# Kernel tuning notes

Measured on AMD Instinct MI355X. Metric: run time of the kernel, lower is better.

## Reference

```python
import jax, jax.numpy as jnp
import numpy as np


def _gcn_conv(x, src, dst, W, b, n_nodes):
    # PyG GCNConv: add self-loops, symmetric deg^{-1/2} normalization, then linear.
    xw = x @ W  # [N, H]
    # degree including self-loop (count of incoming edges at dst + 1)
    deg = jnp.zeros((n_nodes,), dtype=xw.dtype).at[dst].add(1.0) + 1.0
    dinv = jax.lax.rsqrt(deg)  # deg >= 1 always
    coef = (dinv[src] * dinv[dst])[:, None]  # [E, 1]
    out = jnp.zeros_like(xw).at[dst].add(xw[src] * coef)
    # self-loop edge i->i has norm dinv[i]^2
    out = out + xw * (dinv * dinv)[:, None]
    return out + b


def setup_inputs() -> dict:
    key = jax.random.key(0)
    ks = jax.random.split(key, 6)
    N, E, F, H, G = 200000, 600000, 128, 128, 64
    x = jax.random.normal(ks[0], (N, F), dtype=jnp.float32)
    edge_index = jax.random.randint(ks[1], (2, E), 0, N, dtype=jnp.int64)
    batch = jnp.sort(jax.random.randint(ks[2], (N,), 0, G, dtype=jnp.int64))
    W1 = jax.random.normal(ks[3], (F, H), dtype=jnp.float32) * (1.0 / np.sqrt(F))
    b1 = jnp.zeros((H,), dtype=jnp.float32)
    W2 = jax.random.normal(ks[4], (H, H), dtype=jnp.float32) * (1.0 / np.sqrt(H))
    b2 = jnp.zeros((H,), dtype=jnp.float32)
    return {"x": x, "edge_index": edge_index, "batch": batch, "num_graphs": G,
            "W1": W1, "b1": b1, "W2": W2, "b2": b2}


def reference(x, edge_index, batch, num_graphs, W1, b1, W2, b2):
    n_nodes = x.shape[0]
    # feature standardization (torch .std is unbiased, ddof=1)
    x = (x - x.mean(axis=0, keepdims=True)) / x.std(axis=0, keepdims=True, ddof=1)
    src, dst = edge_index[0], edge_index[1]
    h = jax.nn.relu(_gcn_conv(x, src, dst, W1, b1, n_nodes))
    # dropout p=0 -> identity
    h = jax.nn.relu(_gcn_conv(h, src, dst, W2, b2, n_nodes))
    # global_add_pool over batch ids
    return jax.ops.segment_sum(h, batch, num_segments=num_graphs)
```

## Files before the change

kernel.cpp:

```cpp
#include <hip/hip_runtime.h>

#define FDIM 128

typedef __attribute__((ext_vector_type(8))) short short8;
typedef __attribute__((ext_vector_type(4))) float f32x4;

__device__ inline unsigned short f2bf(float f) {
    unsigned int u = __float_as_uint(f);
    unsigned int r = u + 0x7FFFu + ((u >> 16) & 1u);
    return (unsigned short)(r >> 16);
}
__device__ inline float bf2f(unsigned short b) {
    return __uint_as_float((unsigned int)b << 16);
}
__device__ inline void bf8_fma(short8 v, float c, float* acc) {
#pragma unroll
    for (int k = 0; k < 8; ++k)
        acc[k] = fmaf(bf2f(((const unsigned short*)&v)[k]), c, acc[k]);
}

__global__ __launch_bounds__(256) void col_stats_kernel(const float* __restrict__ x, int N,
                                                        float* __restrict__ partials) {
    const int c4 = threadIdx.x & 31;
    const int rg = threadIdx.x >> 5;
    float4 s = make_float4(0.f, 0.f, 0.f, 0.f);
    float4 q = make_float4(0.f, 0.f, 0.f, 0.f);
    for (long r = (long)blockIdx.x * 8 + rg; r < N; r += (long)gridDim.x * 8) {
        float4 v = ((const float4*)x)[r * 32 + c4];
        s.x += v.x; s.y += v.y; s.z += v.z; s.w += v.w;
        q.x += v.x * v.x; q.y += v.y * v.y; q.z += v.z * v.z; q.w += v.w * v.w;
    }
    __shared__ float red[8][32][8];
    float* p = red[rg][c4];
    p[0] = s.x; p[1] = s.y; p[2] = s.z; p[3] = s.w;
    p[4] = q.x; p[5] = q.y; p[6] = q.z; p[7] = q.w;
    __syncthreads();
    if (rg == 0) {
#pragma unroll
        for (int g = 1; g < 8; ++g) {
            const float* o = red[g][c4];
#pragma unroll
            for (int j = 0; j < 8; ++j) red[0][c4][j] += o[j];
        }
        const float* r0 = red[0][c4];
        float* out = &partials[(size_t)blockIdx.x * 256];
        ((float4*)out)[c4] = make_float4(r0[0], r0[1], r0[2], r0[3]);
        ((float4*)(out + 128))[c4] = make_float4(r0[4], r0[5], r0[6], r0[7]);
    }
}

__global__ __launch_bounds__(1024) void finalize_stats(const float* __restrict__ partials,
                                                       int nblk, int N,
                                                       float* __restrict__ mean,
                                                       float* __restrict__ rstd) {
    __shared__ float sh[8][2][FDIM];
    int g = threadIdx.x >> 7;
    int j = threadIdx.x & 127;
    float s = 0.f, q = 0.f;
    for (int b = g; b < nblk; b += 8) {
        s += partials[(size_t)b * 256 + j];
        q += partials[(size_t)b * 256 + 128 + j];
    }
    sh[g][0][j] = s;
    sh[g][1][j] = q;
    __syncthreads();
    if (g == 0) {
#pragma unroll
        for (int k = 1; k < 8; ++k) { s += sh[k][0][j]; q += sh[k][1][j]; }
        float m = s / (float)N;
        float var = (q - (float)N * m * m) / (float)(N - 1);
        mean[j] = m;
        rstd[j] = rsqrtf(var);
    }
}

__global__ void prep_wt(const float* __restrict__ W1, const float* __restrict__ W2,
                        const float* __restrict__ mean, const float* __restrict__ rstd,
                        unsigned short* __restrict__ WT1, unsigned short* __restrict__ WT2,
                        float* __restrict__ bias0) {
    int h = threadIdx.x;
    int b = blockIdx.x;
    if (b < 8) {
        float acc = 0.f;
#pragma unroll
        for (int jj = 0; jj < 16; ++jj) {
            int j = b * 16 + jj;
            float w = W1[j * FDIM + h] * rstd[j];
            WT1[h * FDIM + j] = f2bf(w);
            acc += mean[j] * w;
        }
        unsafeAtomicAdd(&bias0[h], -acc);
    } else {
#pragma unroll
        for (int jj = 0; jj < 16; ++jj) {
            int j = (b - 8) * 16 + jj;
            WT2[h * FDIM + j] = f2bf(W2[j * FDIM + h]);
        }
    }
}

__global__ void deg_count(const int* __restrict__ dst, int E, int* __restrict__ cnt) {
    int e = blockIdx.x * blockDim.x + threadIdx.x;
    if (e < E) atomicAdd(&cnt[dst[e]], 1);
}

__global__ __launch_bounds__(256) void alloc_offsets(const int* __restrict__ cnt, int N,
                                                     int* __restrict__ start,
                                                     int* __restrict__ wcur,
                                                     int* __restrict__ counter,
                                                     float* __restrict__ dinv) {
    __shared__ int sh[256];
    __shared__ int base;
    int i = blockIdx.x * 256 + threadIdx.x;
    int v = (i < N) ? cnt[i] : 0;
    sh[threadIdx.x] = v;
    __syncthreads();
    for (int off = 1; off < 256; off <<= 1) {
        int t = (threadIdx.x >= off) ? sh[threadIdx.x - off] : 0;
        __syncthreads();
        sh[threadIdx.x] += t;
        __syncthreads();
    }
    if (threadIdx.x == 255) base = atomicAdd(counter, sh[255]);
    __syncthreads();
    int excl = base + sh[threadIdx.x] - v;
    if (i < N) {
        start[i] = excl;
        wcur[i] = excl;
        dinv[i] = rsqrtf((float)v + 1.0f);
    }
}

__global__ void fill_edges(const int* __restrict__ src, const int* __restrict__ dst,
                           const float* __restrict__ dinv, int E,
                           int* __restrict__ wcur, int2* __restrict__ edata) {
    int e = blockIdx.x * blockDim.x + threadIdx.x;
    if (e >= E) return;
    int s = src[e], d = dst[e];
    int pos = atomicAdd(&wcur[d], 1);
    edata[pos] = make_int2(s, __float_as_int(dinv[s] * dinv[d]));
}

template <typename T>
__global__ __launch_bounds__(256) void gemm_mfma(const T* __restrict__ A,
                                                 const unsigned short* __restrict__ WT,
                                                 const float* __restrict__ bias,
                                                 unsigned short* __restrict__ C, int M) {
    constexpr int LDA = 136;
    __shared__ unsigned short Alds[64 * LDA];
    __shared__ unsigned short Wlds[FDIM * LDA];
    const int tid = threadIdx.x;
    const int row0 = blockIdx.x * 64;

    for (int i = tid; i < FDIM * 16; i += 256) {
        int r = i >> 4, g = i & 15;
        *(int4*)&Wlds[r * LDA + g * 8] = *(const int4*)&WT[r * FDIM + g * 8];
    }
    if constexpr (sizeof(T) == 4) {
        for (int i = tid; i < 64 * 32; i += 256) {
            int r = i >> 5, c4 = i & 31;
            int row = row0 + r;
            float4 v = make_float4(0.f, 0.f, 0.f, 0.f);
            if (row < M) v = ((const float4*)A)[(size_t)row * 32 + c4];
            ushort4 p;
            p.x = f2bf(v.x); p.y = f2bf(v.y); p.z = f2bf(v.z); p.w = f2bf(v.w);
            *(ushort4*)&Alds[r * LDA + c4 * 4] = p;
        }
    } else {
        for (int i = tid; i < 64 * 16; i += 256) {
            int r = i >> 4, g = i & 15;
            int row = row0 + r;
            int4 v = make_int4(0, 0, 0, 0);
            if (row < M) v = *(const int4*)&A[(size_t)row * FDIM + g * 8];
            *(int4*)&Alds[r * LDA + g * 8] = v;
        }
    }
    __syncthreads();

    const int lane = tid & 63;
    const int wave = tid >> 6;
    const int m16 = lane & 15;
    const int quad = lane >> 4;

    f32x4 acc[8];
#pragma unroll
    for (int t = 0; t < 8; ++t) acc[t] = (f32x4){0.f, 0.f, 0.f, 0.f};

    const unsigned short* Abase = &Alds[(wave * 16 + m16) * LDA + quad * 8];
    const unsigned short* Wbase = &Wlds[m16 * LDA + quad * 8];
#pragma unroll
    for (int s = 0; s < 4; ++s) {
        short8 a = *(const short8*)&Abase[s * 32];
#pragma unroll
        for (int t = 0; t < 8; ++t) {
            short8 b = *(const short8*)&Wbase[t * 16 * LDA + s * 32];
            acc[t] = __builtin_amdgcn_mfma_f32_16x16x32_bf16(a, b, acc[t], 0, 0, 0);
        }
    }

#pragma unroll
    for (int t = 0; t < 8; ++t) {
        float bv = bias ? bias[t * 16 + m16] : 0.f;
#pragma unroll
        for (int i = 0; i < 4; ++i) {
            int r = row0 + wave * 16 + quad * 4 + i;
            if (r < M) C[(size_t)r * FDIM + t * 16 + m16] = f2bf(acc[t][i] + bv);
        }
    }
}

__global__ __launch_bounds__(256) void aggregate(const unsigned short* __restrict__ xw,
                                                 const float* __restrict__ dinv,
                                                 const int* __restrict__ start,
                                                 const int* __restrict__ cnt,
                                                 const int2* __restrict__ edata,
                                                 const float* __restrict__ bvec,
                                                 unsigned short* __restrict__ out, int N) {
    int node = blockIdx.x * 16 + (threadIdx.x >> 4);
    if (node >= N) return;
    const int l8 = threadIdx.x & 15;
    float dv = dinv[node];
    float d2 = dv * dv;
    float4 b0 = ((const float4*)bvec)[l8 * 2];
    float4 b1 = ((const float4*)bvec)[l8 * 2 + 1];
    float acc[8] = {b0.x, b0.y, b0.z, b0.w, b1.x, b1.y, b1.z, b1.w};
    short8 sv = *(const short8*)&xw[(size_t)node * FDIM + l8 * 8];
    bf8_fma(sv, d2, acc);

    int j = start[node];
    const int s1 = j + cnt[node];
    for (; j + 4 <= s1; j += 4) {
        int2 e0 = edata[j], e1 = edata[j + 1], e2 = edata[j + 2], e3 = edata[j + 3];
        short8 u0 = *(const short8*)&xw[(size_t)e0.x * FDIM + l8 * 8];
        short8 u1 = *(const short8*)&xw[(size_t)e1.x * FDIM + l8 * 8];
        short8 u2 = *(const short8*)&xw[(size_t)e2.x * FDIM + l8 * 8];
        short8 u3 = *(const short8*)&xw[(size_t)e3.x * FDIM + l8 * 8];
        bf8_fma(u0, __int_as_float(e0.y), acc);
        bf8_fma(u1, __int_as_float(e1.y), acc);
        bf8_fma(u2, __int_as_float(e2.y), acc);
        bf8_fma(u3, __int_as_float(e3.y), acc);
    }
    for (; j < s1; ++j) {
        int2 ed = edata[j];
        short8 u = *(const short8*)&xw[(size_t)ed.x * FDIM + l8 * 8];
        bf8_fma(u, __int_as_float(ed.y), acc);
    }

    short8 o;
#pragma unroll
    for (int k = 0; k < 8; ++k)
        ((unsigned short*)&o)[k] = f2bf(fmaxf(acc[k], 0.f));
    *(short8*)&out[(size_t)node * FDIM + l8 * 8] = o;
}

#define POOL_ROWS 32
__global__ __launch_bounds__(256) void pool_kernel(const unsigned short* __restrict__ h,
                                                   const int* __restrict__ batch,
                                                   float* __restrict__ out, int N) {
    int unit = blockIdx.x * 4 + (threadIdx.x >> 6);
    int lane = threadIdx.x & 63;
    long r0 = (long)unit * POOL_ROWS;
    if (r0 >= N) return;
    long r1 = min(r0 + (long)POOL_ROWS, (long)N);
    int g0 = batch[r0];
    int g1 = batch[r1 - 1];
    if (g0 == g1) {
        float a0 = 0.f, a1 = 0.f;
#pragma unroll
        for (int i = 0; i < POOL_ROWS; ++i) {
            long r = r0 + i;
            if (r < r1) {
                unsigned int v = *(const unsigned int*)&h[r * FDIM + lane * 2];
                a0 += bf2f((unsigned short)(v & 0xFFFF));
                a1 += bf2f((unsigned short)(v >> 16));
            }
        }
        unsafeAtomicAdd(&out[g0 * FDIM + lane * 2], a0);
        unsafeAtomicAdd(&out[g0 * FDIM + lane * 2 + 1], a1);
    } else {
        float a0 = 0.f, a1 = 0.f;
        int curg = g0;
        for (long r = r0; r < r1; ++r) {
            int g = batch[r];
            if (g != curg) {
                unsafeAtomicAdd(&out[curg * FDIM + lane * 2], a0);
                unsafeAtomicAdd(&out[curg * FDIM + lane * 2 + 1], a1);
                a0 = a1 = 0.f;
                curg = g;
            }
            unsigned int v = *(const unsigned int*)&h[r * FDIM + lane * 2];
            a0 += bf2f((unsigned short)(v & 0xFFFF));
            a1 += bf2f((unsigned short)(v >> 16));
        }
        unsafeAtomicAdd(&out[curg * FDIM + lane * 2], a0);
        unsafeAtomicAdd(&out[curg * FDIM + lane * 2 + 1], a1);
    }
}

extern "C" void kernel_launch(void* const* d_in, const int* in_sizes, int n_in,
                              void* d_out, int out_size, void* d_ws, size_t ws_size,
                              hipStream_t stream) {
    const float* x = (const float*)d_in[0];
    const int* ei = (const int*)d_in[1];
    const int* batch = (const int*)d_in[2];
    const float* W1 = (const float*)d_in[4];
    const float* b1 = (const float*)d_in[5];
    const float* W2 = (const float*)d_in[6];
    const float* b2 = (const float*)d_in[7];

    const int N = in_sizes[2];
    const int E = in_sizes[1] / 2;
    const int* srcp = ei;
    const int* dstp = ei + E;

    const size_t NF = (size_t)N * FDIM;
    unsigned short* bufA = (unsigned short*)d_ws;
    unsigned short* bufB = bufA + NF;
    int* cnt = (int*)(bufB + NF);
    int* counter = cnt + N;
    float* bias0 = (float*)(counter + 4);
    float* dinv = bias0 + FDIM;
    int* start = (int*)(dinv + N);
    int* wcur = start + N;
    float* mean = (float*)(wcur + N);
    float* rstd = mean + FDIM;
    unsigned short* WT1 = (unsigned short*)(rstd + FDIM);
    unsigned short* WT2 = WT1 + FDIM * FDIM;
    int2* edata = (int2*)(WT2 + FDIM * FDIM);
    float* partials = (float*)edata;
    const int STAT_BLOCKS = 512;

    hipMemsetAsync(cnt, 0, ((size_t)N + 4 + FDIM) * sizeof(int), stream);
    hipMemsetAsync(d_out, 0, (size_t)out_size * sizeof(float), stream);

    col_stats_kernel<<<STAT_BLOCKS, 256, 0, stream>>>(x, N, partials);
    finalize_stats<<<1, 1024, 0, stream>>>(partials, STAT_BLOCKS, N, mean, rstd);
    prep_wt<<<16, FDIM, 0, stream>>>(W1, W2, mean, rstd, WT1, WT2, bias0);
    deg_count<<<(E + 255) / 256, 256, 0, stream>>>(dstp, E, cnt);
    alloc_offsets<<<(N + 255) / 256, 256, 0, stream>>>(cnt, N, start, wcur, counter, dinv);
    fill_edges<<<(E + 255) / 256, 256, 0, stream>>>(srcp, dstp, dinv, E, wcur, edata);

    const int gemmGrid = (N + 63) / 64;
    const int aggGrid = (N + 15) / 16;

    gemm_mfma<float><<<gemmGrid, 256, 0, stream>>>(x, WT1, bias0, bufA, N);
    aggregate<<<aggGrid, 256, 0, stream>>>(bufA, dinv, start, cnt, edata, b1, bufB, N);

    gemm_mfma<unsigned short><<<gemmGrid, 256, 0, stream>>>(bufB, WT2, nullptr, bufA, N);
    aggregate<<<aggGrid, 256, 0, stream>>>(bufA, dinv, start, cnt, edata, b2, bufB, N);

    const int poolUnits = (N + POOL_ROWS - 1) / POOL_ROWS;
    pool_kernel<<<(poolUnits + 3) / 4, 256, 0, stream>>>(bufB, batch, (float*)d_out, N);
}
```

Measured before the change: 449.9 us.

## Fuse global pooling into final aggregate and merge small setup kernels

Folds the degree count into the column-stats kernel and merges stats finalization with the weight-transpose prep. The separate pooling kernel is removed: the second aggregate now reduces its ReLU outputs per block in shared memory and atomically adds them to the graph output. This avoids writing and re-reading the final hidden buffer and cuts several launches. In exchange it adds shared-memory atomics and a block barrier in the aggregate kernel.

```diff
diff --git a/kernel.cpp b/kernel.cpp
--- a/kernel.cpp
+++ b/kernel.cpp
@@ -19,13 +19,20 @@
         acc[k] = fmaf(bf2f(((const unsigned short*)&v)[k]), c, acc[k]);
 }
 
-__global__ __launch_bounds__(256) void col_stats_kernel(const float* __restrict__ x, int N,
-                                                        float* __restrict__ partials) {
+__global__ __launch_bounds__(256) void pre_combo(const float* __restrict__ x, int N,
+                                                 float* __restrict__ partials, int statBlocks,
+                                                 const int* __restrict__ dst, int E,
+                                                 int* __restrict__ cnt) {
+    if ((int)blockIdx.x >= statBlocks) {
+        int e = (blockIdx.x - statBlocks) * 256 + threadIdx.x;
+        if (e < E) atomicAdd(&cnt[dst[e]], 1);
+        return;
+    }
     const int c4 = threadIdx.x & 31;
     const int rg = threadIdx.x >> 5;
     float4 s = make_float4(0.f, 0.f, 0.f, 0.f);
     float4 q = make_float4(0.f, 0.f, 0.f, 0.f);
-    for (long r = (long)blockIdx.x * 8 + rg; r < N; r += (long)gridDim.x * 8) {
+    for (long r = (long)blockIdx.x * 8 + rg; r < N; r += (long)statBlocks * 8) {
         float4 v = ((const float4*)x)[r * 32 + c4];
         s.x += v.x; s.y += v.y; s.z += v.z; s.w += v.w;
         q.x += v.x * v.x; q.y += v.y * v.y; q.z += v.z * v.z; q.w += v.w * v.w;
@@ -49,59 +56,55 @@
     }
 }
 
-__global__ __launch_bounds__(1024) void finalize_stats(const float* __restrict__ partials,
-                                                       int nblk, int N,
-                                                       float* __restrict__ mean,
-                                                       float* __restrict__ rstd) {
-    __shared__ float sh[8][2][FDIM];
-    int g = threadIdx.x >> 7;
-    int j = threadIdx.x & 127;
+__global__ __launch_bounds__(256) void stats_prep(const float* __restrict__ partials,
+                                                  int nblk, int N,
+                                                  const float* __restrict__ W1,
+                                                  const float* __restrict__ W2,
+                                                  unsigned short* __restrict__ WT1,
+                                                  unsigned short* __restrict__ WT2,
+                                                  float* __restrict__ bias0) {
+    __shared__ float mean_sh[FDIM], rstd_sh[FDIM];
+    __shared__ float red[2][2][FDIM];
+    const int half = threadIdx.x >> 7;
+    const int j = threadIdx.x & 127;
     float s = 0.f, q = 0.f;
-    for (int b = g; b < nblk; b += 8) {
+    for (int b = half; b < nblk; b += 2) {
         s += partials[(size_t)b * 256 + j];
         q += partials[(size_t)b * 256 + 128 + j];
     }
-    sh[g][0][j] = s;
-    sh[g][1][j] = q;
-    __syncthreads();
-    if (g == 0) {
-#pragma unroll
-        for (int k = 1; k < 8; ++k) { s += sh[k][0][j]; q += sh[k][1][j]; }
+    red[half][0][j] = s;
+    red[half][1][j] = q;
+    __syncthreads();
+    if (half == 0) {
+        s += red[1][0][j];
+        q += red[1][1][j];
         float m = s / (float)N;
         float var = (q - (float)N * m * m) / (float)(N - 1);
-        mean[j] = m;
-        rstd[j] = rsqrtf(var);
-    }
-}
-
-__global__ void prep_wt(const float* __restrict__ W1, const float* __restrict__ W2,
-                        const float* __restrict__ mean, const float* __restrict__ rstd,
-                        unsigned short* __restrict__ WT1, unsigned short* __restrict__ WT2,
-                        float* __restrict__ bias0) {
-    int h = threadIdx.x;
-    int b = blockIdx.x;
+        mean_sh[j] = m;
+        rstd_sh[j] = rsqrtf(var);
+    }
+    __syncthreads();
+
+    const int b = blockIdx.x;
+    const int h = j;
+    const int jbase0 = (threadIdx.x >> 7) * 8;
     if (b < 8) {
         float acc = 0.f;
 #pragma unroll
-        for (int jj = 0; jj < 16; ++jj) {
-            int j = b * 16 + jj;
-            float w = W1[j * FDIM + h] * rstd[j];
-            WT1[h * FDIM + j] = f2bf(w);
-            acc += mean[j] * w;
+        for (int jj = 0; jj < 8; ++jj) {
+            int j2 = b * 16 + jbase0 + jj;
+            float w = W1[j2 * FDIM + h] * rstd_sh[j2];
+            WT1[h * FDIM + j2] = f2bf(w);
+            acc += mean_sh[j2] * w;
         }
         unsafeAtomicAdd(&bias0[h], -acc);
     } else {
 #pragma unroll
-        for (int jj = 0; jj < 16; ++jj) {
-            int j = (b - 8) * 16 + jj;
-            WT2[h * FDIM + j] = f2bf(W2[j * FDIM + h]);
-        }
-    }
-}
-
-__global__ void deg_count(const int* __restrict__ dst, int E, int* __restrict__ cnt) {
-    int e = blockIdx.x * blockDim.x + threadIdx.x;
-    if (e < E) atomicAdd(&cnt[dst[e]], 1);
+        for (int jj = 0; jj < 8; ++jj) {
+            int j2 = (b - 8) * 16 + jbase0 + jj;
+            WT2[h * FDIM + j2] = f2bf(W2[j2 * FDIM + h]);
+        }
+    }
 }
 
 __global__ __launch_bounds__(256) void alloc_offsets(const int* __restrict__ cnt, int N,
@@ -209,26 +212,36 @@
     }
 }
 
+template <bool POOL>
 __global__ __launch_bounds__(256) void aggregate(const unsigned short* __restrict__ xw,
                                                  const float* __restrict__ dinv,
                                                  const int* __restrict__ start,
                                                  const int* __restrict__ cnt,
                                                  const int2* __restrict__ edata,
                                                  const float* __restrict__ bvec,
-                                                 unsigned short* __restrict__ out, int N) {
-    int node = blockIdx.x * 16 + (threadIdx.x >> 4);
-    if (node >= N) return;
+                                                 unsigned short* __restrict__ out,
+                                                 const int* __restrict__ batch,
+                                                 float* __restrict__ pooled, int N) {
+    __shared__ float pool_sh[FDIM];
+    if (POOL && threadIdx.x < FDIM) pool_sh[threadIdx.x] = 0.f;
+    if (POOL) __syncthreads();
+
+    const int base = blockIdx.x * 16;
+    const int node = base + (threadIdx.x >> 4);
     const int l8 = threadIdx.x & 15;
-    float dv = dinv[node];
+    const bool active = node < N;
+    const int nidx = active ? node : (N - 1);
+
+    float dv = dinv[nidx];
     float d2 = dv * dv;
     float4 b0 = ((const float4*)bvec)[l8 * 2];
     float4 b1 = ((const float4*)bvec)[l8 * 2 + 1];
     float acc[8] = {b0.x, b0.y, b0.z, b0.w, b1.x, b1.y, b1.z, b1.w};
-    short8 sv = *(const short8*)&xw[(size_t)node * FDIM + l8 * 8];
+    short8 sv = *(const short8*)&xw[(size_t)nidx * FDIM + l8 * 8];
     bf8_fma(sv, d2, acc);
 
-    int j = start[node];
-    const int s1 = j + cnt[node];
+    int j = start[nidx];
+    const int s1 = j + (active ? cnt[nidx] : 0);
     for (; j + 4 <= s1; j += 4) {
         int2 e0 = edata[j], e1 = edata[j + 1], e2 = edata[j + 2], e3 = edata[j + 3];
         short8 u0 = *(const short8*)&xw[(size_t)e0.x * FDIM + l8 * 8];
@@ -246,54 +259,34 @@
         bf8_fma(u, __int_as_float(ed.y), acc);
     }
 
-    short8 o;
-#pragma unroll
-    for (int k = 0; k < 8; ++k)
-        ((unsigned short*)&o)[k] = f2bf(fmaxf(acc[k], 0.f));
-    *(short8*)&out[(size_t)node * FDIM + l8 * 8] = o;
-}
-
-#define POOL_ROWS 32
-__global__ __launch_bounds__(256) void pool_kernel(const unsigned short* __restrict__ h,
-                                                   const int* __restrict__ batch,
-                                                   float* __restrict__ out, int N) {
-    int unit = blockIdx.x * 4 + (threadIdx.x >> 6);
-    int lane = threadIdx.x & 63;
-    long r0 = (long)unit * POOL_ROWS;
-    if (r0 >= N) return;
-    long r1 = min(r0 + (long)POOL_ROWS, (long)N);
-    int g0 = batch[r0];
-    int g1 = batch[r1 - 1];
-    if (g0 == g1) {
-        float a0 = 0.f, a1 = 0.f;
-#pragma unroll
-        for (int i = 0; i < POOL_ROWS; ++i) {
-            long r = r0 + i;
-            if (r < r1) {
-                unsigned int v = *(const unsigned int*)&h[r * FDIM + lane * 2];
-                a0 += bf2f((unsigned short)(v & 0xFFFF));
-                a1 += bf2f((unsigned short)(v >> 16));
+    if (!POOL) {
+        short8 o;
+#pragma unroll
+        for (int k = 0; k < 8; ++k)
+            ((unsigned short*)&o)[k] = f2bf(fmaxf(acc[k], 0.f));
+        if (active) *(short8*)&out[(size_t)node * FDIM + l8 * 8] = o;
+    } else {
+        float r[8];
+#pragma unroll
+        for (int k = 0; k < 8; ++k) r[k] = fmaxf(acc[k], 0.f);
+        int g0 = batch[base];
+        int g1 = batch[min(base + 15, N - 1)];
+        if (g0 == g1) {
+            if (active) {
+#pragma unroll
+                for (int k = 0; k < 8; ++k) atomicAdd(&pool_sh[l8 * 8 + k], r[k]);
             }
-        }
-        unsafeAtomicAdd(&out[g0 * FDIM + lane * 2], a0);
-        unsafeAtomicAdd(&out[g0 * FDIM + lane * 2 + 1], a1);
-    } else {
-        float a0 = 0.f, a1 = 0.f;
-        int curg = g0;
-        for (long r = r0; r < r1; ++r) {
-            int g = batch[r];
-            if (g != curg) {
-                unsafeAtomicAdd(&out[curg * FDIM + lane * 2], a0);
-                unsafeAtomicAdd(&out[curg * FDIM + lane * 2 + 1], a1);
-                a0 = a1 = 0.f;
-                curg = g;
+            __syncthreads();
+            if (threadIdx.x < FDIM)
+                unsafeAtomicAdd(&pooled[g0 * FDIM + threadIdx.x], pool_sh[threadIdx.x]);
+        } else {
+            if (active) {
+                int g = batch[node];
+#pragma unroll
+                for (int k = 0; k < 8; ++k)
+                    unsafeAtomicAdd(&pooled[g * FDIM + l8 * 8 + k], r[k]);
             }
-            unsigned int v = *(const unsigned int*)&h[r * FDIM + lane * 2];
-            a0 += bf2f((unsigned short)(v & 0xFFFF));
-            a1 += bf2f((unsigned short)(v >> 16));
-        }
-        unsafeAtomicAdd(&out[curg * FDIM + lane * 2], a0);
-        unsafeAtomicAdd(&out[curg * FDIM + lane * 2 + 1], a1);
+        }
     }
 }
 
@@ -322,9 +315,7 @@
     float* dinv = bias0 + FDIM;
     int* start = (int*)(dinv + N);
     int* wcur = start + N;
-    float* mean = (float*)(wcur + N);
-    float* rstd = mean + FDIM;
-    unsigned short* WT1 = (unsigned short*)(rstd + FDIM);
+    unsigned short* WT1 = (unsigned short*)(wcur + N);
     unsigned short* WT2 = WT1 + FDIM * FDIM;
     int2* edata = (int2*)(WT2 + FDIM * FDIM);
     float* partials = (float*)edata;
@@ -333,22 +324,21 @@
     hipMemsetAsync(cnt, 0, ((size_t)N + 4 + FDIM) * sizeof(int), stream);
     hipMemsetAsync(d_out, 0, (size_t)out_size * sizeof(float), stream);
 
-    col_stats_kernel<<<STAT_BLOCKS, 256, 0, stream>>>(x, N, partials);
-    finalize_stats<<<1, 1024, 0, stream>>>(partials, STAT_BLOCKS, N, mean, rstd);
-    prep_wt<<<16, FDIM, 0, stream>>>(W1, W2, mean, rstd, WT1, WT2, bias0);
-    deg_count<<<(E + 255) / 256, 256, 0, stream>>>(dstp, E, cnt);
+    const int degBlocks = (E + 255) / 256;
+    pre_combo<<<STAT_BLOCKS + degBlocks, 256, 0, stream>>>(x, N, partials, STAT_BLOCKS,
+                                                           dstp, E, cnt);
+    stats_prep<<<16, 256, 0, stream>>>(partials, STAT_BLOCKS, N, W1, W2, WT1, WT2, bias0);
     alloc_offsets<<<(N + 255) / 256, 256, 0, stream>>>(cnt, N, start, wcur, counter, dinv);
-    fill_edges<<<(E + 255) / 256, 256, 0, stream>>>(srcp, dstp, dinv, E, wcur, edata);
+    fill_edges<<<degBlocks, 256, 0, stream>>>(srcp, dstp, dinv, E, wcur, edata);
 
     const int gemmGrid = (N + 63) / 64;
     const int aggGrid = (N + 15) / 16;
 
     gemm_mfma<float><<<gemmGrid, 256, 0, stream>>>(x, WT1, bias0, bufA, N);
-    aggregate<<<aggGrid, 256, 0, stream>>>(bufA, dinv, start, cnt, edata, b1, bufB, N);
+    aggregate<false><<<aggGrid, 256, 0, stream>>>(bufA, dinv, start, cnt, edata, b1,
+                                                  bufB, nullptr, nullptr, N);
 
     gemm_mfma<unsigned short><<<gemmGrid, 256, 0, stream>>>(bufB, WT2, nullptr, bufA, N);
-    aggregate<<<aggGrid, 256, 0, stream>>>(bufA, dinv, start, cnt, edata, b2, bufB, N);
-
-    const int poolUnits = (N + POOL_ROWS - 1) / POOL_ROWS;
-    pool_kernel<<<(poolUnits + 3) / 4, 256, 0, stream>>>(bufB, batch, (float*)d_out, N);
-}
+    aggregate<true><<<aggGrid, 256, 0, stream>>>(bufA, dinv, start, cnt, edata, b2,
+                                                 nullptr, batch, (float*)d_out, N);
+}
```

New measurement: 583.9 us. +29.8%, slower.
